# Kernel optimization log

Measured on AMD Instinct MI355X. Metric: run time of the kernel, lower is better.

## Reference

```python
import jax, jax.numpy as jnp
import numpy as np

B, N, C, H = 8, 1024, 768, 12
DH = C // H


def setup_inputs() -> dict:
    key = jax.random.key(0)
    k1, k2, k3, k4 = jax.random.split(key, 4)
    x = jax.random.normal(k1, (B, N, C), dtype=jnp.float32)
    mask = jax.random.randint(k2, (B, N), 0, 2, dtype=jnp.int32)
    # torch Linear weights stored transposed; build directly as (in, out)
    w_qkv = jax.random.normal(k3, (C, 3 * C), dtype=jnp.float32) * (C ** -0.5)
    w_proj = jax.random.normal(k4, (C, C), dtype=jnp.float32) * (C ** -0.5)
    b_proj = jnp.zeros((C,), dtype=jnp.float32)
    return {"x": x, "mask": mask, "w_qkv": w_qkv, "w_proj": w_proj, "b_proj": b_proj}


def reference(x, mask, w_qkv, w_proj, b_proj):
    scale = DH ** -0.5
    qkv = (x @ w_qkv).reshape(B, N, 3, H, DH)          # (B,N,3,H,Dh)
    q, k, v = jnp.moveaxis(qkv, 2, 0)                  # each (B,N,H,Dh)
    q = q.transpose(0, 2, 1, 3)                        # (B,H,N,Dh)
    k = k.transpose(0, 2, 1, 3)
    v = v.transpose(0, 2, 1, 3)
    attn = jnp.einsum('bhqd,bhkd->bhqk', q, k) * scale  # (B,H,N,N)
    # mask (B,N) masks key positions for all queries/heads
    attn = jnp.where(mask[:, None, None, :] != 0, -jnp.inf, attn)
    attn = jax.nn.softmax(attn, axis=-1)
    out = jnp.einsum('bhqk,bhkd->bhqd', attn, v)        # (B,H,N,Dh)
    out = out.transpose(0, 2, 1, 3).reshape(B, N, C)
    return out @ w_proj + b_proj
```

## Files before the change

kernel.cpp:

```cpp
#include <hip/hip_runtime.h>
#include <cstdint>
#include <cstddef>

#define Bb   8
#define Nn   1024
#define Ccn  768
#define Hh   12
#define DHn  64
#define Mrows (Bb * Nn)
#define N3C  (3 * Ccn)
#define BHn  (Bb * Hh)

typedef __attribute__((ext_vector_type(8))) short bf16x8;
typedef __attribute__((ext_vector_type(4))) float f32x4;

static __device__ __forceinline__ unsigned short f2bf(float f) {
    unsigned int u = __builtin_bit_cast(unsigned int, f);
    return (unsigned short)((u + 0x7FFFu + ((u >> 16) & 1u)) >> 16);
}
static __device__ __forceinline__ float bf2f(unsigned short s) {
    unsigned int u = ((unsigned int)s) << 16;
    return __builtin_bit_cast(float, u);
}
static __device__ __forceinline__ unsigned pack2bf(float a, float b) {
    unsigned ua = __builtin_bit_cast(unsigned, a) + 0x8000u;
    unsigned ub = __builtin_bit_cast(unsigned, b) + 0x8000u;
    return (ua >> 16) | (ub & 0xFFFF0000u);
}
static __device__ __forceinline__ void glds16(const void* g, void* l) {
    __builtin_amdgcn_global_load_lds((const __attribute__((address_space(1))) void*)g,
                                     (__attribute__((address_space(3))) void*)l,
                                     16, 0, 0);
}

__global__ void convert_x_mask_kernel(const float* __restrict__ x,
                                      unsigned short* __restrict__ xb,
                                      const int* __restrict__ mask,
                                      float* __restrict__ maskneg, int n8) {
    int i = blockIdx.x * blockDim.x + threadIdx.x;
    if (i < Mrows) maskneg[i] = (mask[i] != 0) ? -1.0e9f : 0.0f;
    if (i >= n8) return;
    const f32x4* xp = (const f32x4*)x;
    f32x4 a = xp[2 * i], b = xp[2 * i + 1];
    bf16x8 v;
#pragma unroll
    for (int j = 0; j < 4; ++j) {
        v[j]     = (short)f2bf(a[j]);
        v[4 + j] = (short)f2bf(b[j]);
    }
    ((bf16x8*)xb)[i] = v;
}

__global__ void transpose_w_kernel(const float* __restrict__ W,
                                   unsigned short* __restrict__ WT,
                                   int R, int C) {
    __shared__ float tile[32][33];
    const int c0 = blockIdx.x * 32, r0 = blockIdx.y * 32;
    const int tx = threadIdx.x, ty = threadIdx.y;
#pragma unroll
    for (int i = 0; i < 4; ++i)
        tile[ty + i * 8][tx] = W[(size_t)(r0 + ty + i * 8) * C + c0 + tx];
    __syncthreads();
#pragma unroll
    for (int i = 0; i < 4; ++i)
        WT[(size_t)(c0 + ty + i * 8) * R + r0 + tx] = f2bf(tile[tx][ty + i * 8]);
}

__global__ void transpose_v_kernel(const unsigned short* __restrict__ vb,
                                   unsigned short* __restrict__ vtb) {
    __shared__ unsigned short tile[32][34];
    const int bh = blockIdx.z;
    const int d0 = blockIdx.x * 32, n0 = blockIdx.y * 32;
    const int tx = threadIdx.x, ty = threadIdx.y;
    const unsigned short* src = vb + (size_t)bh * Nn * DHn;
    unsigned short* dst = vtb + (size_t)bh * DHn * Nn;
#pragma unroll
    for (int i = 0; i < 4; ++i)
        tile[ty + i * 8][tx] = src[(size_t)(n0 + ty + i * 8) * DHn + d0 + tx];
    __syncthreads();
#pragma unroll
    for (int i = 0; i < 4; ++i)
        dst[(size_t)(d0 + ty + i * 8) * Nn + n0 + tx] = tile[tx][ty + i * 8];
}

__global__ __launch_bounds__(256) void gemm_qkv_kernel(
    const unsigned short* __restrict__ A,
    const unsigned short* __restrict__ BT,
    unsigned short* __restrict__ qkvb) {
    constexpr int K = Ccn;
    const int bm = blockIdx.x, bn = blockIdx.y;
    const int t = threadIdx.x, wv = t >> 6, l = t & 63;
    const int fr = l & 15, quad = l >> 4;
    const int wm = (wv >> 1) * 64, wn = (wv & 1) * 64;
    __shared__ __align__(16) unsigned short As[128 * 32];
    __shared__ __align__(16) unsigned short Bs[128 * 32];
    const f32x4 zero = {0.f, 0.f, 0.f, 0.f};
    f32x4 acc[4][4];
#pragma unroll
    for (int i = 0; i < 4; ++i)
#pragma unroll
        for (int j = 0; j < 4; ++j) acc[i][j] = zero;

    const int srow = wv * 16 + (l >> 2);
    const int scol_dst = (l & 3) * 8;
    const int scol_src = (((l & 3) ^ ((srow >> 1) & 3)) << 3);
    const unsigned short* Ag = A + (size_t)(bm * 128 + srow) * K + scol_src;
    const unsigned short* Bg = BT + (size_t)(bn * 128 + srow) * K + scol_src;
    unsigned short* Al = &As[srow * 32 + scol_dst];
    unsigned short* Bl = &Bs[srow * 32 + scol_dst];
    const int rsw = ((fr >> 1) & 3);

    for (int k0 = 0; k0 < K; k0 += 32) {
        glds16(Ag, Al);
        glds16(Ag + (size_t)64 * K, Al + 64 * 32);
        glds16(Bg, Bl);
        glds16(Bg + (size_t)64 * K, Bl + 64 * 32);
        Ag += 32; Bg += 32;
        __syncthreads();
        bf16x8 af[4], bfv[4];
#pragma unroll
        for (int i = 0; i < 4; ++i)
            af[i] = *(const bf16x8*)&As[(wm + i * 16 + fr) * 32 + ((quad ^ rsw) << 3)];
#pragma unroll
        for (int i = 0; i < 4; ++i)
            bfv[i] = *(const bf16x8*)&Bs[(wn + i * 16 + fr) * 32 + ((quad ^ rsw) << 3)];
#pragma unroll
        for (int i = 0; i < 4; ++i)
#pragma unroll
            for (int j = 0; j < 4; ++j)
                acc[i][j] = __builtin_amdgcn_mfma_f32_16x16x32_bf16(af[i], bfv[j], acc[i][j], 0, 0, 0);
        __syncthreads();
    }
#pragma unroll
    for (int j = 0; j < 4; ++j) {
        int col = bn * 128 + wn + j * 16 + fr;
        int s = col / Ccn;
        int rem = col - s * Ccn;
        int hh = rem >> 6, d = rem & 63;
#pragma unroll
        for (int i = 0; i < 4; ++i) {
#pragma unroll
            for (int r = 0; r < 4; ++r) {
                int row = bm * 128 + wm + i * 16 + quad * 4 + r;
                int b = row >> 10, nq = row & 1023;
                qkvb[((((size_t)s * Bb + b) * Hh + hh) * Nn + nq) * DHn + d] = f2bf(acc[i][j][r]);
            }
        }
    }
}

__global__ __launch_bounds__(256) void gemm_proj_kernel(
    const unsigned short* __restrict__ A,
    const unsigned short* __restrict__ BT,
    const float* __restrict__ bias,
    float* __restrict__ out) {
    constexpr int K = Ccn;
    const int bm = blockIdx.x, bn = blockIdx.y;
    const int t = threadIdx.x, wv = t >> 6, l = t & 63;
    const int fr = l & 15, quad = l >> 4;
    const int wm = (wv >> 1) * 64, wn = (wv & 1) * 32;
    __shared__ __align__(16) unsigned short As[128 * 32];
    __shared__ __align__(16) unsigned short Bs[64 * 32];
    const f32x4 zero = {0.f, 0.f, 0.f, 0.f};
    f32x4 acc[4][2];
#pragma unroll
    for (int i = 0; i < 4; ++i)
#pragma unroll
        for (int j = 0; j < 2; ++j) acc[i][j] = zero;

    const int srow = wv * 16 + (l >> 2);
    const int scol_dst = (l & 3) * 8;
    const int scol_src = (((l & 3) ^ ((srow >> 1) & 3)) << 3);
    const unsigned short* Ag = A + (size_t)(bm * 128 + srow) * K + scol_src;
    unsigned short* Al = &As[srow * 32 + scol_dst];
    const int rB = t >> 2, cB = t & 3;
    const int bsrc = ((cB ^ ((rB >> 1) & 3)) << 3);
    const unsigned short* Bg = BT + (size_t)(bn * 64 + rB) * K + bsrc;
    unsigned short* Bl = &Bs[rB * 32 + cB * 8];
    const int rsw = ((fr >> 1) & 3);

    for (int k0 = 0; k0 < K; k0 += 32) {
        glds16(Ag, Al);
        glds16(Ag + (size_t)64 * K, Al + 64 * 32);
        glds16(Bg, Bl);
        Ag += 32; Bg += 32;
        __syncthreads();
        bf16x8 af[4], bfv[2];
#pragma unroll
        for (int i = 0; i < 4; ++i)
            af[i] = *(const bf16x8*)&As[(wm + i * 16 + fr) * 32 + ((quad ^ rsw) << 3)];
#pragma unroll
        for (int j = 0; j < 2; ++j)
            bfv[j] = *(const bf16x8*)&Bs[(wn + j * 16 + fr) * 32 + ((quad ^ rsw) << 3)];
#pragma unroll
        for (int i = 0; i < 4; ++i)
#pragma unroll
            for (int j = 0; j < 2; ++j)
                acc[i][j] = __builtin_amdgcn_mfma_f32_16x16x32_bf16(af[i], bfv[j], acc[i][j], 0, 0, 0);
        __syncthreads();
    }
#pragma unroll
    for (int j = 0; j < 2; ++j) {
        int col = bn * 64 + wn + j * 16 + fr;
        float bv = bias[col];
#pragma unroll
        for (int i = 0; i < 4; ++i) {
#pragma unroll
            for (int r = 0; r < 4; ++r) {
                int row = bm * 128 + wm + i * 16 + quad * 4 + r;
                out[(size_t)row * Ccn + col] = acc[i][j][r] + bv;
            }
        }
    }
}

__global__ __launch_bounds__(256, 3) void attn_fused(
    const unsigned short* __restrict__ qkvb,
    const unsigned short* __restrict__ vtb,
    const float* __restrict__ maskneg,
    unsigned short* __restrict__ attnb) {
    const int hb = blockIdx.x, qt = blockIdx.y;
    const int b = hb / Hh, h = hb - b * Hh;
    const int t = threadIdx.x, wv = t >> 6, l = t & 63;
    const int fr = l & 15, quad = l >> 4;
    __shared__ __align__(16) unsigned short Ks[2][64 * 64];
    __shared__ __align__(16) unsigned short VTs[2][64 * 64];
    __shared__ __align__(16) unsigned short Pbuf[4][2][16 * 72];
    const size_t bh = (size_t)b * Hh + h;
    const unsigned short* Qg = qkvb + bh * (Nn * DHn);
    const unsigned short* Kg = qkvb + (BHn + bh) * (Nn * DHn);
    const unsigned short* Vg = vtb + bh * (DHn * Nn);
    const float* Mg = maskneg + b * Nn;
    const int q0 = qt * 128 + wv * 32;

    bf16x8 qf[2][2];
#pragma unroll
    for (int g = 0; g < 2; ++g)
#pragma unroll
        for (int c = 0; c < 2; ++c) {
            bf16x8 raw = *(const bf16x8*)&Qg[(size_t)(q0 + g * 16 + fr) * DHn + c * 32 + quad * 8];
            bf16x8 sc;
#pragma unroll
            for (int j = 0; j < 8; ++j)
                sc[j] = (short)f2bf(bf2f((unsigned short)raw[j]) * 0.125f);
            qf[g][c] = sc;
        }
    const f32x4 zero = {0.f, 0.f, 0.f, 0.f};
    f32x4 o[2][4];
    float rs[2] = {0.f, 0.f};
#pragma unroll
    for (int g = 0; g < 2; ++g)
#pragma unroll
        for (int r = 0; r < 4; ++r) o[g][r] = zero;

    const int srow = wv * 8 + (l >> 3);
    const int lincol = (l & 7) * 8;
    const int swzcol = (((l & 7) ^ (srow & 7)) << 3);

    for (int k0 = 0; k0 < Nn; k0 += 128) {
#pragma unroll
        for (int kh = 0; kh < 2; ++kh) {
            glds16(&Kg[(size_t)(k0 + kh * 64 + srow) * DHn + swzcol], &Ks[kh][srow * 64 + lincol]);
            glds16(&Kg[(size_t)(k0 + kh * 64 + srow + 32) * DHn + swzcol], &Ks[kh][(srow + 32) * 64 + lincol]);
            glds16(&Vg[(size_t)srow * Nn + k0 + kh * 64 + swzcol], &VTs[kh][srow * 64 + lincol]);
            glds16(&Vg[(size_t)(srow + 32) * Nn + k0 + kh * 64 + swzcol], &VTs[kh][(srow + 32) * 64 + lincol]);
        }
        f32x4 ci[2][4];
#pragma unroll
        for (int kh = 0; kh < 2; ++kh)
#pragma unroll
            for (int kt = 0; kt < 4; ++kt)
                ci[kh][kt] = *(const f32x4*)&Mg[k0 + kh * 64 + kt * 16 + quad * 4];
        __syncthreads();

#pragma unroll
        for (int kh = 0; kh < 2; ++kh) {
            bf16x8 kf0[4], kf1[4];
#pragma unroll
            for (int kt = 0; kt < 4; ++kt) {
                int rr = kt * 16 + fr, sw = rr & 7;
                kf0[kt] = *(const bf16x8*)&Ks[kh][rr * 64 + ((quad ^ sw) << 3)];
                kf1[kt] = *(const bf16x8*)&Ks[kh][rr * 64 + (((quad + 4) ^ sw) << 3)];
            }
            f32x4 sg[2][4];
#pragma unroll
            for (int g = 0; g < 2; ++g)
#pragma unroll
                for (int kt = 0; kt < 4; ++kt) {
                    f32x4 s = __builtin_amdgcn_mfma_f32_16x16x32_bf16(kf0[kt], qf[g][0], ci[kh][kt], 0, 0, 0);
                    sg[g][kt] = __builtin_amdgcn_mfma_f32_16x16x32_bf16(kf1[kt], qf[g][1], s, 0, 0, 0);
                }
            bf16x8 vf0[4], vf1[4];
#pragma unroll
            for (int dt = 0; dt < 4; ++dt) {
                int rr = dt * 16 + fr, sw = rr & 7;
                vf0[dt] = *(const bf16x8*)&VTs[kh][rr * 64 + ((quad ^ sw) << 3)];
                vf1[dt] = *(const bf16x8*)&VTs[kh][rr * 64 + (((quad + 4) ^ sw) << 3)];
            }

            unsigned short* Pw = Pbuf[wv][kh];
#pragma unroll
            for (int g = 0; g < 2; ++g) {
#pragma unroll
                for (int kt = 0; kt < 4; ++kt) {
                    float p0 = __expf(sg[g][kt][0]);
                    float p1 = __expf(sg[g][kt][1]);
                    float p2 = __expf(sg[g][kt][2]);
                    float p3 = __expf(sg[g][kt][3]);
                    rs[g] += (p0 + p1) + (p2 + p3);
                    uint2 pk;
                    pk.x = pack2bf(p0, p1);
                    pk.y = pack2bf(p2, p3);
                    *(uint2*)&Pw[fr * 72 + kt * 16 + quad * 4] = pk;
                }
                bf16x8 pa0 = *(const bf16x8*)&Pw[fr * 72 + quad * 8];
                bf16x8 pa1 = *(const bf16x8*)&Pw[fr * 72 + 32 + quad * 8];
#pragma unroll
                for (int dt = 0; dt < 4; ++dt) {
                    f32x4 t0 = __builtin_amdgcn_mfma_f32_16x16x32_bf16(pa0, vf0[dt], o[g][dt], 0, 0, 0);
                    o[g][dt] = __builtin_amdgcn_mfma_f32_16x16x32_bf16(pa1, vf1[dt], t0, 0, 0, 0);
                }
            }
        }
        __syncthreads();
    }
#pragma unroll
    for (int g = 0; g < 2; ++g) {
        float r2 = rs[g] + __shfl_xor(rs[g], 16, 64);
        float rfull = r2 + __shfl_xor(r2, 32, 64);
        float inv[4];
#pragma unroll
        for (int r = 0; r < 4; ++r) {
            float lv = __shfl(rfull, quad * 4 + r, 64);
            inv[r] = (lv > 0.f) ? 1.0f / lv : 0.f;
        }
#pragma unroll
        for (int dt = 0; dt < 4; ++dt)
#pragma unroll
            for (int r = 0; r < 4; ++r) {
                int q = q0 + g * 16 + quad * 4 + r;
                attnb[((size_t)(b * Nn + q) * Hh + h) * DHn + dt * 16 + fr] = f2bf(o[g][dt][r] * inv[r]);
            }
    }
}

#define OFF_XB     0u
#define OFF_WQKVT  12582912u
#define OFF_WPROJT 16121856u
#define OFF_MASKB  17301504u
#define OFF_QKVB   17334272u
#define OFF_VTB    55083008u
#define OFF_ATTNB  67665920u

extern "C" void kernel_launch(void* const* d_in, const int* in_sizes, int n_in,
                              void* d_out, int out_size, void* d_ws, size_t ws_size,
                              hipStream_t stream) {
    const float* x      = (const float*)d_in[0];
    const int*   mask   = (const int*)d_in[1];
    const float* w_qkv  = (const float*)d_in[2];
    const float* w_proj = (const float*)d_in[3];
    const float* b_proj = (const float*)d_in[4];
    float* out = (float*)d_out;
    char* ws = (char*)d_ws;
    unsigned short* xb     = (unsigned short*)(ws + OFF_XB);
    unsigned short* wqkvT  = (unsigned short*)(ws + OFF_WQKVT);
    unsigned short* wprojT = (unsigned short*)(ws + OFF_WPROJT);
    float*          maskng = (float*)(ws + OFF_MASKB);
    unsigned short* qkvb   = (unsigned short*)(ws + OFF_QKVB);
    unsigned short* vtb    = (unsigned short*)(ws + OFF_VTB);
    unsigned short* attnb  = (unsigned short*)(ws + OFF_ATTNB);

    convert_x_mask_kernel<<<dim3(3072), dim3(256), 0, stream>>>(x, xb, mask, maskng, Mrows * Ccn / 8);
    transpose_w_kernel<<<dim3(N3C / 32, Ccn / 32), dim3(32, 8), 0, stream>>>(w_qkv, wqkvT, Ccn, N3C);
    transpose_w_kernel<<<dim3(Ccn / 32, Ccn / 32), dim3(32, 8), 0, stream>>>(w_proj, wprojT, Ccn, Ccn);
    gemm_qkv_kernel<<<dim3(Mrows / 128, N3C / 128), dim3(256), 0, stream>>>(xb, wqkvT, qkvb);
    transpose_v_kernel<<<dim3(DHn / 32, Nn / 32, BHn), dim3(32, 8), 0, stream>>>(
        qkvb + (size_t)2 * BHn * Nn * DHn, vtb);
    attn_fused<<<dim3(BHn, Nn / 128), dim3(256), 0, stream>>>(qkvb, vtb, maskng, attnb);
    gemm_proj_kernel<<<dim3(Mrows / 128, Ccn / 64), dim3(256), 0, stream>>>(attnb, wprojT, b_proj, out);
}
```

Baseline: 208.0 us.

## Double-buffer K/V tiles in attention and merge weight transpose launches

The attention kernel now prefetches the next 64-key K/V tile and its mask values into the alternate LDS buffer while computing on the current one. Before, it loaded 128 keys and then waited at a barrier before any compute. The two weight-transpose kernels are also merged into a single launch that picks the matrix from the block index, saving one kernel launch. The P staging buffer shrinks to a single buffer per wave. The cost is an extra barrier per 64-key step and more live registers, which could lower occupancy.

```diff
diff --git a/kernel.cpp b/kernel.cpp
--- a/kernel.cpp
+++ b/kernel.cpp
@@ -51,11 +51,17 @@
     ((bf16x8*)xb)[i] = v;
 }
 
-__global__ void transpose_w_kernel(const float* __restrict__ W,
-                                   unsigned short* __restrict__ WT,
-                                   int R, int C) {
+__global__ void transpose_w2_kernel(const float* __restrict__ Wqkv,
+                                    unsigned short* __restrict__ WqkvT,
+                                    const float* __restrict__ Wproj,
+                                    unsigned short* __restrict__ WprojT) {
     __shared__ float tile[32][33];
-    const int c0 = blockIdx.x * 32, r0 = blockIdx.y * 32;
+    int xb = blockIdx.x;
+    const float* W; unsigned short* WT; int C;
+    if (xb < 72) { W = Wqkv;  WT = WqkvT;  C = N3C; }
+    else         { W = Wproj; WT = WprojT; C = Ccn; xb -= 72; }
+    const int R = Ccn;
+    const int c0 = xb * 32, r0 = blockIdx.y * 32;
     const int tx = threadIdx.x, ty = threadIdx.y;
 #pragma unroll
     for (int i = 0; i < 4; ++i)
@@ -225,7 +231,7 @@
     const int fr = l & 15, quad = l >> 4;
     __shared__ __align__(16) unsigned short Ks[2][64 * 64];
     __shared__ __align__(16) unsigned short VTs[2][64 * 64];
-    __shared__ __align__(16) unsigned short Pbuf[4][2][16 * 72];
+    __shared__ __align__(16) unsigned short Pbuf[4][16 * 72];
     const size_t bh = (size_t)b * Hh + h;
     const unsigned short* Qg = qkvb + bh * (Nn * DHn);
     const unsigned short* Kg = qkvb + (BHn + bh) * (Nn * DHn);
@@ -257,71 +263,79 @@
     const int lincol = (l & 7) * 8;
     const int swzcol = (((l & 7) ^ (srow & 7)) << 3);
 
+    auto stage = [&](int kbase, int bsel) {
+        glds16(&Kg[(size_t)(kbase + srow) * DHn + swzcol], &Ks[bsel][srow * 64 + lincol]);
+        glds16(&Kg[(size_t)(kbase + srow + 32) * DHn + swzcol], &Ks[bsel][(srow + 32) * 64 + lincol]);
+        glds16(&Vg[(size_t)srow * Nn + kbase + swzcol], &VTs[bsel][srow * 64 + lincol]);
+        glds16(&Vg[(size_t)(srow + 32) * Nn + kbase + swzcol], &VTs[bsel][(srow + 32) * 64 + lincol]);
+    };
+    auto loadci = [&](int kbase, f32x4* ci) {
+#pragma unroll
+        for (int kt = 0; kt < 4; ++kt)
+            ci[kt] = *(const f32x4*)&Mg[kbase + kt * 16 + quad * 4];
+    };
+    auto compute = [&](int bsel, const f32x4* ci) {
+        bf16x8 kf0[4], kf1[4];
+#pragma unroll
+        for (int kt = 0; kt < 4; ++kt) {
+            int rr = kt * 16 + fr, sw = rr & 7;
+            kf0[kt] = *(const bf16x8*)&Ks[bsel][rr * 64 + ((quad ^ sw) << 3)];
+            kf1[kt] = *(const bf16x8*)&Ks[bsel][rr * 64 + (((quad + 4) ^ sw) << 3)];
+        }
+        f32x4 sg[2][4];
+#pragma unroll
+        for (int g = 0; g < 2; ++g)
+#pragma unroll
+            for (int kt = 0; kt < 4; ++kt) {
+                f32x4 s = __builtin_amdgcn_mfma_f32_16x16x32_bf16(kf0[kt], qf[g][0], ci[kt], 0, 0, 0);
+                sg[g][kt] = __builtin_amdgcn_mfma_f32_16x16x32_bf16(kf1[kt], qf[g][1], s, 0, 0, 0);
+            }
+        bf16x8 vf0[4], vf1[4];
+#pragma unroll
+        for (int dt = 0; dt < 4; ++dt) {
+            int rr = dt * 16 + fr, sw = rr & 7;
+            vf0[dt] = *(const bf16x8*)&VTs[bsel][rr * 64 + ((quad ^ sw) << 3)];
+            vf1[dt] = *(const bf16x8*)&VTs[bsel][rr * 64 + (((quad + 4) ^ sw) << 3)];
+        }
+        unsigned short* Pw = Pbuf[wv];
+#pragma unroll
+        for (int g = 0; g < 2; ++g) {
+#pragma unroll
+            for (int kt = 0; kt < 4; ++kt) {
+                float p0 = __expf(sg[g][kt][0]);
+                float p1 = __expf(sg[g][kt][1]);
+                float p2 = __expf(sg[g][kt][2]);
+                float p3 = __expf(sg[g][kt][3]);
+                rs[g] += (p0 + p1) + (p2 + p3);
+                uint2 pk;
+                pk.x = pack2bf(p0, p1);
+                pk.y = pack2bf(p2, p3);
+                *(uint2*)&Pw[fr * 72 + kt * 16 + quad * 4] = pk;
+            }
+            bf16x8 pa0 = *(const bf16x8*)&Pw[fr * 72 + quad * 8];
+            bf16x8 pa1 = *(const bf16x8*)&Pw[fr * 72 + 32 + quad * 8];
+#pragma unroll
+            for (int dt = 0; dt < 4; ++dt) {
+                f32x4 t0 = __builtin_amdgcn_mfma_f32_16x16x32_bf16(pa0, vf0[dt], o[g][dt], 0, 0, 0);
+                o[g][dt] = __builtin_amdgcn_mfma_f32_16x16x32_bf16(pa1, vf1[dt], t0, 0, 0, 0);
+            }
+        }
+    };
+
+    f32x4 ciA[4], ciB[4];
+    stage(0, 0);
+    loadci(0, ciA);
+    __syncthreads();
     for (int k0 = 0; k0 < Nn; k0 += 128) {
-#pragma unroll
-        for (int kh = 0; kh < 2; ++kh) {
-            glds16(&Kg[(size_t)(k0 + kh * 64 + srow) * DHn + swzcol], &Ks[kh][srow * 64 + lincol]);
-            glds16(&Kg[(size_t)(k0 + kh * 64 + srow + 32) * DHn + swzcol], &Ks[kh][(srow + 32) * 64 + lincol]);
-            glds16(&Vg[(size_t)srow * Nn + k0 + kh * 64 + swzcol], &VTs[kh][srow * 64 + lincol]);
-            glds16(&Vg[(size_t)(srow + 32) * Nn + k0 + kh * 64 + swzcol], &VTs[kh][(srow + 32) * 64 + lincol]);
-        }
-        f32x4 ci[2][4];
-#pragma unroll
-        for (int kh = 0; kh < 2; ++kh)
-#pragma unroll
-            for (int kt = 0; kt < 4; ++kt)
-                ci[kh][kt] = *(const f32x4*)&Mg[k0 + kh * 64 + kt * 16 + quad * 4];
-        __syncthreads();
-
-#pragma unroll
-        for (int kh = 0; kh < 2; ++kh) {
-            bf16x8 kf0[4], kf1[4];
-#pragma unroll
-            for (int kt = 0; kt < 4; ++kt) {
-                int rr = kt * 16 + fr, sw = rr & 7;
-                kf0[kt] = *(const bf16x8*)&Ks[kh][rr * 64 + ((quad ^ sw) << 3)];
-                kf1[kt] = *(const bf16x8*)&Ks[kh][rr * 64 + (((quad + 4) ^ sw) << 3)];
-            }
-            f32x4 sg[2][4];
-#pragma unroll
-            for (int g = 0; g < 2; ++g)
-#pragma unroll
-                for (int kt = 0; kt < 4; ++kt) {
-                    f32x4 s = __builtin_amdgcn_mfma_f32_16x16x32_bf16(kf0[kt], qf[g][0], ci[kh][kt], 0, 0, 0);
-                    sg[g][kt] = __builtin_amdgcn_mfma_f32_16x16x32_bf16(kf1[kt], qf[g][1], s, 0, 0, 0);
-                }
-            bf16x8 vf0[4], vf1[4];
-#pragma unroll
-            for (int dt = 0; dt < 4; ++dt) {
-                int rr = dt * 16 + fr, sw = rr & 7;
-                vf0[dt] = *(const bf16x8*)&VTs[kh][rr * 64 + ((quad ^ sw) << 3)];
-                vf1[dt] = *(const bf16x8*)&VTs[kh][rr * 64 + (((quad + 4) ^ sw) << 3)];
-            }
-
-            unsigned short* Pw = Pbuf[wv][kh];
-#pragma unroll
-            for (int g = 0; g < 2; ++g) {
-#pragma unroll
-                for (int kt = 0; kt < 4; ++kt) {
-                    float p0 = __expf(sg[g][kt][0]);
-                    float p1 = __expf(sg[g][kt][1]);
-                    float p2 = __expf(sg[g][kt][2]);
-                    float p3 = __expf(sg[g][kt][3]);
-                    rs[g] += (p0 + p1) + (p2 + p3);
-                    uint2 pk;
-                    pk.x = pack2bf(p0, p1);
-                    pk.y = pack2bf(p2, p3);
-                    *(uint2*)&Pw[fr * 72 + kt * 16 + quad * 4] = pk;
-                }
-                bf16x8 pa0 = *(const bf16x8*)&Pw[fr * 72 + quad * 8];
-                bf16x8 pa1 = *(const bf16x8*)&Pw[fr * 72 + 32 + quad * 8];
-#pragma unroll
-                for (int dt = 0; dt < 4; ++dt) {
-                    f32x4 t0 = __builtin_amdgcn_mfma_f32_16x16x32_bf16(pa0, vf0[dt], o[g][dt], 0, 0, 0);
-                    o[g][dt] = __builtin_amdgcn_mfma_f32_16x16x32_bf16(pa1, vf1[dt], t0, 0, 0, 0);
-                }
-            }
-        }
+        stage(k0 + 64, 1);
+        loadci(k0 + 64, ciB);
+        compute(0, ciA);
+        __syncthreads();
+        if (k0 + 128 < Nn) {
+            stage(k0 + 128, 0);
+            loadci(k0 + 128, ciA);
+        }
+        compute(1, ciB);
         __syncthreads();
     }
 #pragma unroll
@@ -371,8 +385,7 @@
     unsigned short* attnb  = (unsigned short*)(ws + OFF_ATTNB);
 
     convert_x_mask_kernel<<<dim3(3072), dim3(256), 0, stream>>>(x, xb, mask, maskng, Mrows * Ccn / 8);
-    transpose_w_kernel<<<dim3(N3C / 32, Ccn / 32), dim3(32, 8), 0, stream>>>(w_qkv, wqkvT, Ccn, N3C);
-    transpose_w_kernel<<<dim3(Ccn / 32, Ccn / 32), dim3(32, 8), 0, stream>>>(w_proj, wprojT, Ccn, Ccn);
+    transpose_w2_kernel<<<dim3(96, 24), dim3(32, 8), 0, stream>>>(w_qkv, wqkvT, w_proj, wprojT);
     gemm_qkv_kernel<<<dim3(Mrows / 128, N3C / 128), dim3(256), 0, stream>>>(xb, wqkvT, qkvb);
     transpose_v_kernel<<<dim3(DHn / 32, Nn / 32, BHn), dim3(32, 8), 0, stream>>>(
         qkvb + (size_t)2 * BHn * Nn * DHn, vtb);
```

Result: slower. 213.5 us (+2.6%).
